# Kernel optimization log

Hardware: AMD Instinct MI355X
Metric: run time of the kernel (lower is better)

## Reference

```python
import jax, jax.numpy as jnp
import numpy as np

SCALE = 64.0
MARGIN = 0.35
EPS = 1e-12  # torch F.normalize eps


def _l2norm(a, axis):
    n = jnp.sqrt(jnp.sum(a * a, axis=axis, keepdims=True))
    return a / jnp.maximum(n, EPS)


def setup_inputs() -> dict:
    key = jax.random.key(0)
    k1, k2, k3 = jax.random.split(key, 3)
    B, D, C = 512, 512, 100000
    x = jax.random.normal(k1, (B, D), dtype=jnp.float32)
    gt = jax.random.randint(k2, (B,), 0, C, dtype=jnp.int64)
    # kaiming_normal_ on [C, D]: std = sqrt(2 / fan_in) with fan_in = D
    wt = jax.random.normal(k3, (C, D), dtype=jnp.float32) * np.sqrt(2.0 / D)
    return {"x": x, "gt": gt, "wt": wt}


def reference(x, gt, wt):
    wt_norm = _l2norm(wt, axis=1)          # [C, D]
    x_norm = _l2norm(x, axis=1)            # [B, D]
    cos = jnp.einsum("bd,cd->bc", x_norm, wt_norm)  # [B, C]
    # margin only at target index (avoids materializing one-hot)
    b = jnp.arange(x.shape[0])
    margin_score = cos.at[b, gt].add(-MARGIN)
    logits = SCALE * margin_score
    logp = jax.nn.log_softmax(logits, axis=-1)
    nll = -logp[b, gt]
    return jnp.mean(nll)
```

## Files before the change

### kernel.cpp

```cpp
#include <hip/hip_runtime.h>
#include <hip/hip_bf16.h>

#define DIM 512
#define BATCH 512
#define CCLS 100000
#define BM 256
#define BN 128
#define NT 782

typedef __attribute__((ext_vector_type(8))) short bf16x8;
typedef __attribute__((ext_vector_type(4))) float f32x4;

__device__ __forceinline__ unsigned short f2bf(float f) {
  union { float f; unsigned int u; } v; v.f = f;
  unsigned int u = v.u;
  return (unsigned short)((u + 0x7fffu + ((u >> 16) & 1u)) >> 16);
}

__device__ __forceinline__ void async_copy16(const unsigned short* g, unsigned short* l) {
  __builtin_amdgcn_global_load_lds((const __attribute__((address_space(1))) void*)g,
                                   (__attribute__((address_space(3))) void*)l, 16, 0, 0);
}

__global__ __launch_bounds__(256) void rownorm_all(const float* __restrict__ wt,
                                                   const float* __restrict__ x,
                                                   unsigned short* __restrict__ wn,
                                                   unsigned short* __restrict__ xn) {
  int wave = threadIdx.x >> 6;
  int lane = threadIdx.x & 63;
  int row4 = blockIdx.x * 4 + wave;
  const float* in;
  unsigned short* out;
  int row;
  if (row4 < CCLS) { in = wt; out = wn; row = row4; }
  else             { in = x;  out = xn; row = row4 - CCLS; }
  const float4* src = (const float4*)(in + (size_t)row * DIM);
  float4 v0 = src[lane];
  float4 v1 = src[lane + 64];
  float ss = v0.x*v0.x + v0.y*v0.y + v0.z*v0.z + v0.w*v0.w
           + v1.x*v1.x + v1.y*v1.y + v1.z*v1.z + v1.w*v1.w;
  #pragma unroll
  for (int off = 32; off > 0; off >>= 1) ss += __shfl_xor(ss, off, 64);
  float r = 1.0f / fmaxf(sqrtf(ss), 1e-12f);
  ushort4 o0, o1;
  o0.x = f2bf(v0.x * r); o0.y = f2bf(v0.y * r); o0.z = f2bf(v0.z * r); o0.w = f2bf(v0.w * r);
  o1.x = f2bf(v1.x * r); o1.y = f2bf(v1.y * r); o1.z = f2bf(v1.z * r); o1.w = f2bf(v1.w * r);
  ushort4* dst = (ushort4*)(out + (size_t)row * DIM);
  dst[lane]      = o0;
  dst[lane + 64] = o1;
}

__global__ __launch_bounds__(512, 4) void cosface_gemm(
    const unsigned short* __restrict__ xn,
    const unsigned short* __restrict__ wn,
    const int* __restrict__ gt,
    float* __restrict__ partial,
    float* __restrict__ tgt) {
  __shared__ unsigned short lds_a[BM * 64];
  __shared__ unsigned short lds_b[BN * 64];
  __shared__ float lds_rowsum[BM];
  __shared__ int lds_gt[BM];

  const int tid = threadIdx.x;
  const int lane = tid & 63;
  const int w = tid >> 6;
  const int wm = w >> 1;
  const int wn_ = w & 1;
  const int mt = blockIdx.x;
  const int nt = blockIdx.y;

  if (tid < BM) {
    lds_rowsum[tid] = 0.f;
    lds_gt[tid] = gt[mt * BM + tid];
  }

  const unsigned short* ga[4];
  const unsigned short* gb[2];
  #pragma unroll
  for (int j = 0; j < 4; ++j) {
    int c = j * 512 + tid;
    int m = c >> 3;
    int qg = (c & 7) ^ (m & 7);
    ga[j] = xn + (size_t)(mt * BM + m) * DIM + qg * 8;
  }
  #pragma unroll
  for (int j = 0; j < 2; ++j) {
    int c = j * 512 + tid;
    int m = c >> 3;
    int qg = (c & 7) ^ (m & 7);
    int rowB = nt * BN + m;
    if (rowB >= CCLS) rowB = CCLS - 1;
    gb[j] = wn + (size_t)rowB * DIM + qg * 8;
  }

  f32x4 acc[4][4];
  #pragma unroll
  for (int i = 0; i < 4; ++i)
    #pragma unroll
    for (int j = 0; j < 4; ++j)
      acc[i][j] = (f32x4){0.f, 0.f, 0.f, 0.f};

  const int quad = lane >> 4;
  const int l15 = lane & 15;
  const int arow = wm * 64 + l15;
  const int brow = wn_ * 64 + l15;
  const int sw = (l15 & 7);

  for (int kk = 0; kk < 8; ++kk) {
    #pragma unroll
    for (int j = 0; j < 4; ++j)
      async_copy16(ga[j] + kk * 64, &lds_a[(j * 512 + w * 64) * 8]);
    #pragma unroll
    for (int j = 0; j < 2; ++j)
      async_copy16(gb[j] + kk * 64, &lds_b[(j * 512 + w * 64) * 8]);
    __syncthreads();
    #pragma unroll
    for (int s = 0; s < 2; ++s) {
      bf16x8 af[4], bf[4];
      int q = s * 4 + quad;
      int qs = (q ^ sw) * 8;
      #pragma unroll
      for (int i = 0; i < 4; ++i) {
        af[i] = *(const bf16x8*)&lds_a[(arow + i * 16) * 64 + qs];
        bf[i] = *(const bf16x8*)&lds_b[(brow + i * 16) * 64 + qs];
      }
      #pragma unroll
      for (int i = 0; i < 4; ++i)
        #pragma unroll
        for (int j = 0; j < 4; ++j)
          acc[i][j] = __builtin_amdgcn_mfma_f32_16x16x32_bf16(af[i], bf[j], acc[i][j], 0, 0, 0);
    }
    __syncthreads();
  }

  #pragma unroll
  for (int i = 0; i < 4; ++i) {
    #pragma unroll
    for (int reg = 0; reg < 4; ++reg) {
      int m_loc = wm * 64 + i * 16 + quad * 4 + reg;
      int m_g = mt * BM + m_loc;
      int gtm = lds_gt[m_loc];
      float s = 0.f;
      #pragma unroll
      for (int j = 0; j < 4; ++j) {
        int n_g = nt * BN + wn_ * 64 + j * 16 + l15;
        float logit = 64.f * acc[i][j][reg];
        if (n_g == gtm) {
          logit -= 64.f * 0.35f;
          tgt[m_g] = logit;
        }
        if (n_g < CCLS) s += __expf(logit - 64.f);
      }
      #pragma unroll
      for (int off = 1; off < 16; off <<= 1) s += __shfl_xor(s, off, 64);
      if (l15 == 0) atomicAdd(&lds_rowsum[m_loc], s);
    }
  }
  __syncthreads();
  if (tid < BM)
    partial[(size_t)(mt * BM + tid) * NT + nt] = lds_rowsum[tid];
}

__global__ __launch_bounds__(64) void nll_rows(const float* __restrict__ partial,
                                               const float* __restrict__ tgt,
                                               float* __restrict__ nll) {
  int m = blockIdx.x;
  int lane = threadIdx.x;
  const float* row = partial + (size_t)m * NT;
  float s = 0.f;
  for (int t = lane; t < NT; t += 64) s += row[t];
  #pragma unroll
  for (int off = 32; off > 0; off >>= 1) s += __shfl_xor(s, off, 64);
  if (lane == 0) nll[m] = (logf(s) + 64.f) - tgt[m];
}

__global__ __launch_bounds__(512) void reduce_mean(const float* __restrict__ nll,
                                                   float* __restrict__ out) {
  __shared__ float red[BATCH];
  int m = threadIdx.x;
  red[m] = nll[m];
  __syncthreads();
  for (int k = 256; k > 0; k >>= 1) {
    if (m < k) red[m] += red[m + k];
    __syncthreads();
  }
  if (m == 0) out[0] = red[0] * (1.0f / BATCH);
}

extern "C" void kernel_launch(void* const* d_in, const int* in_sizes, int n_in,
                              void* d_out, int out_size, void* d_ws, size_t ws_size,
                              hipStream_t stream) {
  const float* x  = (const float*)d_in[0];
  const int*   gt = (const int*)d_in[1];
  const float* wt = (const float*)d_in[2];
  float* out = (float*)d_out;

  char* ws = (char*)d_ws;
  unsigned short* wn = (unsigned short*)ws;
  unsigned short* xn = (unsigned short*)(ws + 102400000);
  float* partial     = (float*)(ws + 102400000 + 524288);
  float* tgt         = (float*)(ws + 102400000 + 524288 + 1601536);
  float* nll         = (float*)(ws + 102400000 + 524288 + 1601536 + 2048);

  rownorm_all<<<(CCLS + BATCH) / 4, 256, 0, stream>>>(wt, x, wn, xn);
  cosface_gemm<<<dim3(2, NT), 512, 0, stream>>>(xn, wn, gt, partial, tgt);
  nll_rows<<<BATCH, 64, 0, stream>>>(partial, tgt, nll);
  reduce_mean<<<1, BATCH, 0, stream>>>(nll, out);
}
```

Measured before the change: 367.4 us.

## Quantize normalized rows to FP8 and run the cosine GEMM with FP8 MFMA

The row-normalization kernel now writes FP8 (packed through cvt_pk_fp8) instead of BF16. The GEMM loads byte-wide tiles with a matching swizzle and uses the 16x16x32 FP8 MFMA over four K-steps of 128 bytes. This halves the intermediate weight buffer written and re-read, and the bytes moved into LDS. The cost is much coarser precision on the cosine values, which are scaled by 64 into logits, so the loss may drift past tolerance.

```diff
diff --git a/kernel.cpp b/kernel.cpp
--- a/kernel.cpp
+++ b/kernel.cpp
@@ -8,56 +8,48 @@
 #define BN 128
 #define NT 782
 
-typedef __attribute__((ext_vector_type(8))) short bf16x8;
 typedef __attribute__((ext_vector_type(4))) float f32x4;
 
-__device__ __forceinline__ unsigned short f2bf(float f) {
-  union { float f; unsigned int u; } v; v.f = f;
-  unsigned int u = v.u;
-  return (unsigned short)((u + 0x7fffu + ((u >> 16) & 1u)) >> 16);
-}
-
-__device__ __forceinline__ void async_copy16(const unsigned short* g, unsigned short* l) {
+__device__ __forceinline__ void async_copy16(const unsigned char* g, unsigned char* l) {
   __builtin_amdgcn_global_load_lds((const __attribute__((address_space(1))) void*)g,
                                    (__attribute__((address_space(3))) void*)l, 16, 0, 0);
 }
 
-__global__ __launch_bounds__(256) void rownorm_all(const float* __restrict__ wt,
+__global__ __launch_bounds__(256) void rownorm_fp8(const float* __restrict__ wt,
                                                    const float* __restrict__ x,
-                                                   unsigned short* __restrict__ wn,
-                                                   unsigned short* __restrict__ xn) {
+                                                   unsigned char* __restrict__ wn,
+                                                   unsigned char* __restrict__ xn) {
   int wave = threadIdx.x >> 6;
   int lane = threadIdx.x & 63;
   int row4 = blockIdx.x * 4 + wave;
   const float* in;
-  unsigned short* out;
+  unsigned char* out;
   int row;
   if (row4 < CCLS) { in = wt; out = wn; row = row4; }
   else             { in = x;  out = xn; row = row4 - CCLS; }
   const float4* src = (const float4*)(in + (size_t)row * DIM);
-  float4 v0 = src[lane];
-  float4 v1 = src[lane + 64];
+  float4 v0 = src[2 * lane];
+  float4 v1 = src[2 * lane + 1];
   float ss = v0.x*v0.x + v0.y*v0.y + v0.z*v0.z + v0.w*v0.w
            + v1.x*v1.x + v1.y*v1.y + v1.z*v1.z + v1.w*v1.w;
   #pragma unroll
   for (int off = 32; off > 0; off >>= 1) ss += __shfl_xor(ss, off, 64);
   float r = 1.0f / fmaxf(sqrtf(ss), 1e-12f);
-  ushort4 o0, o1;
-  o0.x = f2bf(v0.x * r); o0.y = f2bf(v0.y * r); o0.z = f2bf(v0.z * r); o0.w = f2bf(v0.w * r);
-  o1.x = f2bf(v1.x * r); o1.y = f2bf(v1.y * r); o1.z = f2bf(v1.z * r); o1.w = f2bf(v1.w * r);
-  ushort4* dst = (ushort4*)(out + (size_t)row * DIM);
-  dst[lane]      = o0;
-  dst[lane + 64] = o1;
+  int p0 = __builtin_amdgcn_cvt_pk_fp8_f32(v0.x * r, v0.y * r, 0, false);
+  p0     = __builtin_amdgcn_cvt_pk_fp8_f32(v0.z * r, v0.w * r, p0, true);
+  int p1 = __builtin_amdgcn_cvt_pk_fp8_f32(v1.x * r, v1.y * r, 0, false);
+  p1     = __builtin_amdgcn_cvt_pk_fp8_f32(v1.z * r, v1.w * r, p1, true);
+  ((int2*)(out + (size_t)row * DIM))[lane] = make_int2(p0, p1);
 }
 
 __global__ __launch_bounds__(512, 4) void cosface_gemm(
-    const unsigned short* __restrict__ xn,
-    const unsigned short* __restrict__ wn,
+    const unsigned char* __restrict__ xn,
+    const unsigned char* __restrict__ wn,
     const int* __restrict__ gt,
     float* __restrict__ partial,
     float* __restrict__ tgt) {
-  __shared__ unsigned short lds_a[BM * 64];
-  __shared__ unsigned short lds_b[BN * 64];
+  __shared__ __align__(16) unsigned char lds_a[BM * 128];
+  __shared__ __align__(16) unsigned char lds_b[BN * 128];
   __shared__ float lds_rowsum[BM];
   __shared__ int lds_gt[BM];
 
@@ -74,14 +66,14 @@
     lds_gt[tid] = gt[mt * BM + tid];
   }
 
-  const unsigned short* ga[4];
-  const unsigned short* gb[2];
+  const unsigned char* ga[4];
+  const unsigned char* gb[2];
   #pragma unroll
   for (int j = 0; j < 4; ++j) {
     int c = j * 512 + tid;
     int m = c >> 3;
     int qg = (c & 7) ^ (m & 7);
-    ga[j] = xn + (size_t)(mt * BM + m) * DIM + qg * 8;
+    ga[j] = xn + (size_t)(mt * BM + m) * DIM + qg * 16;
   }
   #pragma unroll
   for (int j = 0; j < 2; ++j) {
@@ -90,7 +82,7 @@
     int qg = (c & 7) ^ (m & 7);
     int rowB = nt * BN + m;
     if (rowB >= CCLS) rowB = CCLS - 1;
-    gb[j] = wn + (size_t)rowB * DIM + qg * 8;
+    gb[j] = wn + (size_t)rowB * DIM + qg * 16;
   }
 
   f32x4 acc[4][4];
@@ -104,31 +96,33 @@
   const int l15 = lane & 15;
   const int arow = wm * 64 + l15;
   const int brow = wn_ * 64 + l15;
-  const int sw = (l15 & 7);
-
-  for (int kk = 0; kk < 8; ++kk) {
+  const int swA = arow & 7;
+  const int swB = brow & 7;
+
+  for (int kk = 0; kk < 4; ++kk) {
     #pragma unroll
     for (int j = 0; j < 4; ++j)
-      async_copy16(ga[j] + kk * 64, &lds_a[(j * 512 + w * 64) * 8]);
+      async_copy16(ga[j] + kk * 128, &lds_a[(j * 512 + w * 64) * 16]);
     #pragma unroll
     for (int j = 0; j < 2; ++j)
-      async_copy16(gb[j] + kk * 64, &lds_b[(j * 512 + w * 64) * 8]);
+      async_copy16(gb[j] + kk * 128, &lds_b[(j * 512 + w * 64) * 16]);
     __syncthreads();
     #pragma unroll
-    for (int s = 0; s < 2; ++s) {
-      bf16x8 af[4], bf[4];
-      int q = s * 4 + quad;
-      int qs = (q ^ sw) * 8;
+    for (int s = 0; s < 4; ++s) {
+      int g = s * 4 + quad;
+      int cs = g >> 1;
+      int h = (g & 1) * 8;
+      long long af[4], bf[4];
       #pragma unroll
       for (int i = 0; i < 4; ++i) {
-        af[i] = *(const bf16x8*)&lds_a[(arow + i * 16) * 64 + qs];
-        bf[i] = *(const bf16x8*)&lds_b[(brow + i * 16) * 64 + qs];
+        af[i] = *(const long long*)&lds_a[(arow + i * 16) * 128 + ((cs ^ swA) * 16) + h];
+        bf[i] = *(const long long*)&lds_b[(brow + i * 16) * 128 + ((cs ^ swB) * 16) + h];
       }
       #pragma unroll
       for (int i = 0; i < 4; ++i)
         #pragma unroll
         for (int j = 0; j < 4; ++j)
-          acc[i][j] = __builtin_amdgcn_mfma_f32_16x16x32_bf16(af[i], bf[j], acc[i][j], 0, 0, 0);
+          acc[i][j] = __builtin_amdgcn_mfma_f32_16x16x32_fp8_fp8(af[i], bf[j], acc[i][j], 0, 0, 0);
     }
     __syncthreads();
   }
@@ -196,13 +190,13 @@
   float* out = (float*)d_out;
 
   char* ws = (char*)d_ws;
-  unsigned short* wn = (unsigned short*)ws;
-  unsigned short* xn = (unsigned short*)(ws + 102400000);
-  float* partial     = (float*)(ws + 102400000 + 524288);
-  float* tgt         = (float*)(ws + 102400000 + 524288 + 1601536);
-  float* nll         = (float*)(ws + 102400000 + 524288 + 1601536 + 2048);
-
-  rownorm_all<<<(CCLS + BATCH) / 4, 256, 0, stream>>>(wt, x, wn, xn);
+  unsigned char* wn = (unsigned char*)ws;
+  unsigned char* xn = (unsigned char*)(ws + 51200000);
+  float* partial    = (float*)(ws + 51462144);
+  float* tgt        = (float*)(ws + 53063680);
+  float* nll        = (float*)(ws + 53065728);
+
+  rownorm_fp8<<<(CCLS + BATCH) / 4, 256, 0, stream>>>(wt, x, wn, xn);
   cosface_gemm<<<dim3(2, NT), 512, 0, stream>>>(xn, wn, gt, partial, tgt);
   nll_rows<<<BATCH, 64, 0, stream>>>(partial, tgt, nll);
   reduce_mean<<<1, BATCH, 0, stream>>>(nll, out);
```

After: 348.7 us. 5.1% less time.
